# Performance work log

Measured on AMD Instinct MI355X. Metric: run time of the kernel, lower is better.

Reference implementation:

```python
import jax, jax.numpy as jnp
import numpy as np
import math

EMBED = 1024
HEADS = 16
HEAD_DIM = EMBED // HEADS  # 64
BSZ = 32
TGT = 512   # == src_len, required by the bmm-over-sequence structure
SRC = 512   # == BSZ*HEADS, required by the need_weights view


def _xavier(k, shape):
    fan_out, fan_in = shape
    limit = math.sqrt(6.0 / (fan_in + fan_out))
    return jax.random.uniform(k, shape, jnp.float32, -limit, limit)


def setup_inputs() -> dict:
    key = jax.random.key(0)
    ks = jax.random.split(key, 8)
    d = EMBED
    return {
        # query given as [bsz, tgt_len, d]; the module transposes it internally
        "query": jax.random.normal(ks[0], (BSZ, TGT, d), jnp.float32),
        "key": jax.random.normal(ks[1], (SRC, BSZ, d), jnp.float32),
        "value": jax.random.normal(ks[2], (SRC, BSZ, d), jnp.float32),
        "Wq": _xavier(ks[3], (d, d)), "bq": jnp.zeros((d,), jnp.float32),
        "Wk": _xavier(ks[4], (d, d)), "bk": jnp.zeros((d,), jnp.float32),
        "Wv": _xavier(ks[5], (d, d)), "bv": jnp.zeros((d,), jnp.float32),
        "Wo": _xavier(ks[6], (d, d)), "bo": jnp.zeros((d,), jnp.float32),
    }


def reference(query, key, value, Wq, bq, Wk, bk, Wv, bv, Wo, bo):
    H, hd = HEADS, HEAD_DIM
    # module transposes [bsz, tgt_len, d] -> [tgt_len, bsz, d]
    query = jnp.transpose(query, (1, 0, 2))
    T, B, D = query.shape
    S = key.shape[0]  # == T and == B*H by construction
    # projections (nn.Linear: x @ W.T + b)
    q = (query @ Wq.T + bq).reshape(T, B * H, hd)
    k = (key @ Wk.T + bk).reshape(S, B * H, hd)
    v = (value @ Wv.T + bv).reshape(S, B * H, hd)
    # torch.bmm with the SEQUENCE dim as the bmm batch dim (faithful to source):
    # scores: [T, BH, BH]
    scores = jnp.einsum('tbd,tcd->tbc', q, k) / jnp.sqrt(jnp.asarray(hd, q.dtype))
    attn = jax.nn.softmax(scores, axis=-1)  # dropout p=0.0, eval mode
    out = jnp.einsum('tbc,tcd->tbd', attn, v)  # [T, BH, hd]
    out = out.reshape(T, B, D) @ Wo.T + bo     # [T, B, D]
    # need_weights=True branch: view [T,H,B,S], permute(2,1,0,3), mean over heads
    w = attn.reshape(T, H, B, S).transpose(2, 1, 0, 3).mean(axis=1)  # [B, T, S]
    return out, w
```

## Files before the change

kernel.cpp:

```cpp
#include <hip/hip_runtime.h>
#include <hip/hip_bf16.h>
#include <stdint.h>


typedef __attribute__((ext_vector_type(8))) short bf16x8;
typedef __attribute__((ext_vector_type(4))) float f32x4;
typedef unsigned short u16;
typedef unsigned int u32;

typedef __attribute__((address_space(1))) const unsigned int as1_u32;
typedef __attribute__((address_space(3))) unsigned int as3_u32;

__device__ __forceinline__ void glds16(const void* g, void* l) {
    __builtin_amdgcn_global_load_lds((as1_u32*)g, (as3_u32*)l, 16, 0, 0);
}

__device__ __forceinline__ u16 f2bf(float f) {
    u32 u = __builtin_bit_cast(u32, f);
    u32 r = (u + 0x7FFFu + ((u >> 16) & 1u)) >> 16;
    return (u16)r;
}

template <int CTRL>
__device__ __forceinline__ float dpp_add(float x) {
    int xi = __builtin_bit_cast(int, x);
    int yi = __builtin_amdgcn_update_dpp(0, xi, CTRL, 0xF, 0xF, true);
    return x + __builtin_bit_cast(float, yi);
}
__device__ __forceinline__ float red16(float v) {
    v = dpp_add<0xB1>(v);
    v = dpp_add<0x4E>(v);
    v = dpp_add<0x141>(v);
    v = dpp_add<0x140>(v);
    return v;
}

__global__ void convw_kernel(const float4* __restrict__ query,
                             const float4* __restrict__ key,
                             const float4* __restrict__ value,
                             const float4* __restrict__ Wq, const float4* __restrict__ Wk,
                             const float4* __restrict__ Wv, const float4* __restrict__ Wo,
                             uint2* __restrict__ qx, uint2* __restrict__ kx,
                             uint2* __restrict__ vx,
                             uint2* __restrict__ wqb, uint2* __restrict__ wkb,
                             uint2* __restrict__ wvb, uint2* __restrict__ wob) {
    const int NT = gridDim.x * blockDim.x;
    for (int i = blockIdx.x * blockDim.x + threadIdx.x; i < 13631488; i += NT) {
        float4 v; uint2* d; int di;
        if (i < 4194304) {
            int m = i >> 8, c4 = i & 255;
            int t = m >> 5, b = m & 31;
            v = query[(b * 512 + t) * 256 + c4];
            d = qx; di = i;
        } else if (i < 8388608) {
            di = i - 4194304; v = key[di]; d = kx;
        } else if (i < 12582912) {
            di = i - 8388608; v = value[di]; d = vx;
        } else {
            int jj = i - 12582912;
            int wsel = jj >> 18; di = jj & 262143;
            const float4* s = wsel == 0 ? Wq : wsel == 1 ? Wk : wsel == 2 ? Wv : Wo;
            d = wsel == 0 ? wqb : wsel == 1 ? wkb : wsel == 2 ? wvb : wob;
            v = s[di];
        }
        uint2 r;
        r.x = (u32)f2bf(v.x) | ((u32)f2bf(v.y) << 16);
        r.y = (u32)f2bf(v.z) | ((u32)f2bf(v.w) << 16);
        d[di] = r;
    }
}

template <int F32OUT>
__global__ __launch_bounds__(256, 2)
void gemm_bb(const u16* __restrict__ A0, const u16* __restrict__ A1,
             const u16* __restrict__ A2,
             const u16* __restrict__ B0, const u16* __restrict__ B1,
             const u16* __restrict__ B2,
             const float* __restrict__ b0, const float* __restrict__ b1,
             const float* __restrict__ b2,
             void* __restrict__ C0, void* __restrict__ C1, void* __restrict__ C2) {
    __shared__ __align__(16) u16 As[2][8192];
    __shared__ __align__(16) u16 Bs[2][8192];
    const int z = blockIdx.z;
    const u16* A = z == 0 ? A0 : z == 1 ? A1 : A2;
    const u16* B = z == 0 ? B0 : z == 1 ? B1 : B2;
    const float* bias = z == 0 ? b0 : z == 1 ? b1 : b2;
    void* Cp = z == 0 ? C0 : z == 1 ? C1 : C2;
    const int tid = threadIdx.x;
    const int id = blockIdx.x;
    const int xcd = id & 7, j = id >> 3;
    const int ny = j & 7, band = xcd * 16 + (j >> 3);
    const long N0 = (long)ny * 128;
    const long M0 = (long)band * 128;
    const int lane = tid & 63, wv = tid >> 6;
    const int l15 = lane & 15, g = lane >> 4;
    const int wm = (wv >> 1) * 64, wn = (wv & 1) * 64;

    auto gldsAB = [&](int kt, int buf) {
#pragma unroll
        for (int i2 = 0; i2 < 4; ++i2) {
            int q = tid + 256 * i2; int r = q >> 3, c16 = q & 7;
            int c16s = c16 ^ (r & 7);
            char* lbA = (char*)As[buf] + (i2 * 256 + wv * 64) * 16;
            char* lbB = (char*)Bs[buf] + (i2 * 256 + wv * 64) * 16;
            glds16(A + (M0 + r) * 1024 + kt * 64 + c16s * 8, lbA);
            glds16(B + (N0 + r) * 1024 + kt * 64 + c16s * 8, lbB);
        }
    };
    gldsAB(0, 0);
    __syncthreads();
    f32x4 acc[4][4] = {};
    const int swz = (l15 & 7) << 4;
    for (int kt = 0; kt < 16; ++kt) {
        if (kt < 15) gldsAB(kt + 1, (kt + 1) & 1);
        const char* Acur = (const char*)As[kt & 1];
        const char* Bcur = (const char*)Bs[kt & 1];
#pragma unroll
        for (int kk = 0; kk < 2; ++kk) {
            bf16x8 av[4], bvv[4];
#pragma unroll
            for (int mt = 0; mt < 4; ++mt) {
                int row = wm + mt * 16 + l15;
                av[mt] = *(const bf16x8*)(Acur + row * 128 + ((kk * 64 + g * 16) ^ swz));
            }
#pragma unroll
            for (int nt = 0; nt < 4; ++nt) {
                int row = wn + nt * 16 + l15;
                bvv[nt] = *(const bf16x8*)(Bcur + row * 128 + ((kk * 64 + g * 16) ^ swz));
            }
#pragma unroll
            for (int mt = 0; mt < 4; ++mt)
#pragma unroll
                for (int nt = 0; nt < 4; ++nt)
                    acc[mt][nt] = __builtin_amdgcn_mfma_f32_16x16x32_bf16(av[mt], bvv[nt], acc[mt][nt], 0, 0, 0);
        }
        __syncthreads();
    }
    float bsv[4];
#pragma unroll
    for (int nt = 0; nt < 4; ++nt) bsv[nt] = bias[N0 + wn + nt * 16 + l15];
#pragma unroll
    for (int mt = 0; mt < 4; ++mt)
#pragma unroll
        for (int nt = 0; nt < 4; ++nt)
#pragma unroll
            for (int r = 0; r < 4; ++r) {
                long m = M0 + wm + mt * 16 + g * 4 + r;
                long n = N0 + wn + nt * 16 + l15;
                float v = acc[mt][nt][r] + bsv[nt];
                if (F32OUT) ((float*)Cp)[m * 1024 + n] = v;
                else        ((u16*)Cp)[m * 1024 + n] = f2bf(v);
            }
}

__global__ __launch_bounds__(512, 2)
void attn_kernel(const u16* __restrict__ Q, const u16* __restrict__ K,
                 const u16* __restrict__ V, u16* __restrict__ ctx,
                 float* __restrict__ wout) {
    __shared__ __align__(16) char smem[32768];
    const int bid = blockIdx.x;
    const int wk_ = (bid & 7) * 256 + (bid >> 3);
    const int t = wk_ >> 2, it = wk_ & 3;
    const int tid = threadIdx.x, lane = tid & 63, wv = tid >> 6;
    const int l15 = lane & 15, g = lane >> 4;
    const int swk = (l15 & 7) << 4;
    const int bb = it * 8 + wv;
    const float ksc = 0.18033688011112042f;

    const u16* Kt = K + (size_t)t * 32768;
    const u16* Vt = V + (size_t)t * 32768;

    auto stageK = [&](int q, int slot) {
#pragma unroll
        for (int hh = 0; hh < 2; ++hh) {
            int idx = hh * 512 + tid;
            int sl = idx >> 3, c16 = idx & 7;
            int csw = c16 ^ (sl & 7);
            glds16(Kt + (size_t)(q * 128 + sl) * 64 + csw * 8,
                   smem + slot * 16384 + hh * 8192 + wv * 1024);
        }
    };
    bf16x8 vreg[2];
    auto loadV = [&](int q) {
#pragma unroll
        for (int hh = 0; hh < 2; ++hh) {
            int u = hh * 512 + tid;
            int sl = u >> 3, ec = u & 7;
            vreg[hh] = *(const bf16x8*)(Vt + (size_t)(q * 128 + sl) * 64 + ec * 8);
        }
    };
    auto writeV = [&](int slot) {
        char* base = smem + slot * 16384;
#pragma unroll
        for (int hh = 0; hh < 2; ++hh) {
            int u = hh * 512 + tid;
            int sl = u >> 3, ec = u & 7;
#pragma unroll
            for (int jj = 0; jj < 8; ++jj) {
                int swv = (jj ^ (ec & 3)) << 4;
                *(u16*)(base + (ec * 8 + jj) * 256 + ((sl * 2) ^ swv)) = (u16)vreg[hh][jj];
            }
        }
    };
    f32x4 pv[4];
    auto pvQuarter = [&](const char* vb, bf16x8 p0, bf16x8 p1, bf16x8 p2, bf16x8 p3) {
        bf16x8 pq[4] = {p0, p1, p2, p3};
        __builtin_amdgcn_s_setprio(1);
#pragma unroll
        for (int m = 0; m < 4; ++m) {
#pragma unroll
            for (int nt = 0; nt < 4; ++nt) {
                int e = nt * 16 + l15;
                int esw = ((e & 7) ^ ((e >> 3) & 3)) << 4;
                const char* vrow = vb + e * 256;
                union { bf16x8 v; uint2 uu[2]; } bv;
                bv.uu[0] = *(const uint2*)(vrow + ((m * 64 + 8 * g) ^ esw));
                bv.uu[1] = *(const uint2*)(vrow + ((m * 64 + 32 + 8 * g) ^ esw));
                pv[nt] = __builtin_amdgcn_mfma_f32_16x16x32_bf16(pq[m], bv.v, pv[nt], 0, 0, 0);
            }
        }
        __builtin_amdgcn_s_setprio(0);
    };

    const int c = 32 * l15 + bb;
    const u16* qrow = Q + ((size_t)t * 512 + c) * 64;
    bf16x8 qb0 = *(const bf16x8*)(qrow + g * 8);
    bf16x8 qb1 = *(const bf16x8*)(qrow + 32 + g * 8);

    stageK(0, 0);
    __syncthreads();
    float sum = 0.f;
    bf16x8 pP[16];
#pragma unroll
    for (int q = 0; q < 4; ++q) {
        if (q < 3) stageK(q + 1, (q + 1) & 1);
        else loadV(0);
        const char* kb = smem + (q & 1) * 16384;
        __builtin_amdgcn_s_setprio(1);
#pragma unroll
        for (int m = 0; m < 4; ++m) {
            union { bf16x8 v; u32 u[4]; } pa;
#pragma unroll
            for (int h2 = 0; h2 < 2; ++h2) {
                int lsl = 2 * m + h2;
                const char* rowp = kb + (lsl * 16 + l15) * 128;
                bf16x8 a0 = *(const bf16x8*)(rowp + ((g * 16) ^ swk));
                bf16x8 a1 = *(const bf16x8*)(rowp + ((64 + g * 16) ^ swk));
                f32x4 zz = {0.f, 0.f, 0.f, 0.f};
                zz = __builtin_amdgcn_mfma_f32_16x16x32_bf16(a0, qb0, zz, 0, 0, 0);
                zz = __builtin_amdgcn_mfma_f32_16x16x32_bf16(a1, qb1, zz, 0, 0, 0);
                float e0 = exp2f(zz[0] * ksc), e1 = exp2f(zz[1] * ksc);
                float e2 = exp2f(zz[2] * ksc), e3 = exp2f(zz[3] * ksc);
                sum += (e0 + e1) + (e2 + e3);
                pa.u[2 * h2]     = (u32)f2bf(e0) | ((u32)f2bf(e1) << 16);
                pa.u[2 * h2 + 1] = (u32)f2bf(e2) | ((u32)f2bf(e3) << 16);
            }
            pP[q * 4 + m] = pa.v;
        }
        __builtin_amdgcn_s_setprio(0);
        __syncthreads();
    }
    sum += __shfl_xor(sum, 16);
    sum += __shfl_xor(sum, 32);
    const float inv = 1.f / sum;

    writeV(0);
    loadV(1);

    {
        const float inv16 = inv * 0.0625f;
        float4 wreg0 = {0.f, 0.f, 0.f, 0.f}, wreg1 = {0.f, 0.f, 0.f, 0.f};
#pragma unroll
        for (int st = 0; st < 32; ++st) {
            union { bf16x8 v; u32 u[4]; } pu; pu.v = pP[st >> 1];
            u32 ua = pu.u[(st & 1) * 2], ub = pu.u[(st & 1) * 2 + 1];
            float v0 = __builtin_bit_cast(float, (ua & 0xFFFFu) << 16) * inv16;
            float v1 = __builtin_bit_cast(float, ua & 0xFFFF0000u) * inv16;
            float v2 = __builtin_bit_cast(float, (ub & 0xFFFFu) << 16) * inv16;
            float v3 = __builtin_bit_cast(float, ub & 0xFFFF0000u) * inv16;
            v0 = red16(v0); v1 = red16(v1); v2 = red16(v2); v3 = red16(v3);
            if ((st >> 1) == l15) {
                if (st & 1) wreg1 = (float4){v0, v1, v2, v3};
                else        wreg0 = (float4){v0, v1, v2, v3};
            }
        }
        float* wrow = wout + ((size_t)(bb * 512 + t)) * 512 + 32 * l15 + 4 * g;
        *(float4*)(wrow) = wreg0;
        *(float4*)(wrow + 16) = wreg1;
    }
    __syncthreads();

#pragma unroll
    for (int nt = 0; nt < 4; ++nt) pv[nt] = (f32x4){0.f, 0.f, 0.f, 0.f};
    writeV(1);
    pvQuarter(smem, pP[0], pP[1], pP[2], pP[3]);
    loadV(2);
    __syncthreads();
    writeV(0);
    pvQuarter(smem + 16384, pP[4], pP[5], pP[6], pP[7]);
    loadV(3);
    __syncthreads();
    writeV(1);
    pvQuarter(smem, pP[8], pP[9], pP[10], pP[11]);
    __syncthreads();
    pvQuarter(smem + 16384, pP[12], pP[13], pP[14], pP[15]);

    float invv[4];
#pragma unroll
    for (int r = 0; r < 4; ++r) invv[r] = __shfl(inv, g * 4 + r);
#pragma unroll
    for (int nt = 0; nt < 4; ++nt)
#pragma unroll
        for (int r = 0; r < 4; ++r)
            ctx[((size_t)t * 512 + 32 * (g * 4 + r) + bb) * 64 + nt * 16 + l15] =
                f2bf(pv[nt][r] * invv[r]);
}

extern "C" void kernel_launch(void* const* d_in, const int* in_sizes, int n_in,
                              void* d_out, int out_size, void* d_ws, size_t ws_size,
                              hipStream_t stream) {
    const float* query = (const float*)d_in[0];
    const float* key   = (const float*)d_in[1];
    const float* value = (const float*)d_in[2];
    const float* Wq = (const float*)d_in[3];  const float* bq = (const float*)d_in[4];
    const float* Wk = (const float*)d_in[5];  const float* bk = (const float*)d_in[6];
    const float* Wv = (const float*)d_in[7];  const float* bv = (const float*)d_in[8];
    const float* Wo = (const float*)d_in[9];  const float* bo = (const float*)d_in[10];

    char* ws = (char*)d_ws;
    u16* wqb  = (u16*)(ws + 0);
    u16* wkb  = (u16*)(ws + 2097152);
    u16* wvb  = (u16*)(ws + 4194304);
    u16* wob  = (u16*)(ws + 6291456);
    u16* q_ws = (u16*)(ws + 8388608);
    u16* k_ws = (u16*)(ws + 41943040);
    u16* v_ws = (u16*)(ws + 75497472);
    u16* qx   = (u16*)(ws + 109051904);

    float* out  = (float*)d_out;
    float* wout = out + 16777216;
    u16* kx = (u16*)d_out;
    u16* vx = (u16*)((char*)d_out + 33554432);

    convw_kernel<<<2048, 256, 0, stream>>>(
        (const float4*)query, (const float4*)key, (const float4*)value,
        (const float4*)Wq, (const float4*)Wk, (const float4*)Wv, (const float4*)Wo,
        (uint2*)qx, (uint2*)kx, (uint2*)vx,
        (uint2*)wqb, (uint2*)wkb, (uint2*)wvb, (uint2*)wob);

    dim3 gg3(1024, 1, 3);
    gemm_bb<0><<<gg3, 256, 0, stream>>>(qx, kx, vx, wqb, wkb, wvb,
                                        bq, bk, bv, q_ws, k_ws, v_ws);

    attn_kernel<<<2048, 512, 0, stream>>>(q_ws, k_ws, v_ws, q_ws, wout);

    gemm_bb<1><<<dim3(1024, 1, 1), 256, 0, stream>>>(q_ws, q_ws, q_ws,
                                                     wob, wob, wob, bo, bo, bo,
                                                     out, out, out);
}
```

Baseline: 353.8 us.

## Pre-transpose V in a separate kernel and stage it via async LDS loads

Adds a kernel that transposes the V projection per sequence position into an [e][c] layout in a scratch region of the output buffer. The attention kernel can then stage V tiles with global_load_lds 16-byte copies, replacing the register load followed by scalar 2-byte scattered LDS writes, and the V-slot swizzle is simplified to match. The aim is to cut LDS write instruction count and register pressure in the attention kernel. In exchange it adds an extra kernel launch plus a full read and write of V (32 MB bf16) through global memory.

```diff
diff --git a/kernel.cpp b/kernel.cpp
--- a/kernel.cpp
+++ b/kernel.cpp
@@ -153,9 +153,33 @@
             }
 }
 
+__global__ __launch_bounds__(256)
+void vtrans_kernel(const u16* __restrict__ v_ws, u16* __restrict__ vt) {
+    __shared__ __align__(16) u16 tl[64][136];
+    const int bid = blockIdx.x;
+    const int t = bid >> 2, c0 = (bid & 3) * 128;
+    const u16* src = v_ws + (size_t)t * 32768 + (size_t)c0 * 64;
+#pragma unroll
+    for (int i = 0; i < 4; ++i) {
+        int ch = i * 256 + threadIdx.x;
+        int rc = ch >> 3, e0 = (ch & 7) * 8;
+        bf16x8 v8 = *(const bf16x8*)(src + rc * 64 + e0);
+#pragma unroll
+        for (int j = 0; j < 8; ++j) tl[e0 + j][rc] = (u16)v8[j];
+    }
+    __syncthreads();
+    u16* dst = vt + (size_t)t * 32768 + c0;
+#pragma unroll
+    for (int i = 0; i < 4; ++i) {
+        int ch = i * 256 + threadIdx.x;
+        int e = ch >> 4, cc = (ch & 15) * 8;
+        *(bf16x8*)(dst + (size_t)e * 512 + cc) = *(const bf16x8*)(&tl[e][cc]);
+    }
+}
+
 __global__ __launch_bounds__(512, 2)
 void attn_kernel(const u16* __restrict__ Q, const u16* __restrict__ K,
-                 const u16* __restrict__ V, u16* __restrict__ ctx,
+                 const u16* __restrict__ VT, u16* __restrict__ ctx,
                  float* __restrict__ wout) {
     __shared__ __align__(16) char smem[32768];
     const int bid = blockIdx.x;
@@ -168,7 +192,7 @@
     const float ksc = 0.18033688011112042f;
 
     const u16* Kt = K + (size_t)t * 32768;
-    const u16* Vt = V + (size_t)t * 32768;
+    const u16* Vtt = VT + (size_t)t * 32768;
 
     auto stageK = [&](int q, int slot) {
 #pragma unroll
@@ -180,26 +204,13 @@
                    smem + slot * 16384 + hh * 8192 + wv * 1024);
         }
     };
-    bf16x8 vreg[2];
-    auto loadV = [&](int q) {
+    auto stageV = [&](int q, int slot) {
 #pragma unroll
         for (int hh = 0; hh < 2; ++hh) {
-            int u = hh * 512 + tid;
-            int sl = u >> 3, ec = u & 7;
-            vreg[hh] = *(const bf16x8*)(Vt + (size_t)(q * 128 + sl) * 64 + ec * 8);
-        }
-    };
-    auto writeV = [&](int slot) {
-        char* base = smem + slot * 16384;
-#pragma unroll
-        for (int hh = 0; hh < 2; ++hh) {
-            int u = hh * 512 + tid;
-            int sl = u >> 3, ec = u & 7;
-#pragma unroll
-            for (int jj = 0; jj < 8; ++jj) {
-                int swv = (jj ^ (ec & 3)) << 4;
-                *(u16*)(base + (ec * 8 + jj) * 256 + ((sl * 2) ^ swv)) = (u16)vreg[hh][jj];
-            }
+            int ch = hh * 512 + tid;
+            int e = ch >> 4, c16 = ch & 15;
+            glds16(Vtt + (size_t)e * 512 + q * 128 + ((c16 ^ (e & 7)) << 3),
+                   smem + slot * 16384 + hh * 8192 + wv * 1024);
         }
     };
     f32x4 pv[4];
@@ -211,7 +222,7 @@
 #pragma unroll
             for (int nt = 0; nt < 4; ++nt) {
                 int e = nt * 16 + l15;
-                int esw = ((e & 7) ^ ((e >> 3) & 3)) << 4;
+                int esw = (e & 7) << 4;
                 const char* vrow = vb + e * 256;
                 union { bf16x8 v; uint2 uu[2]; } bv;
                 bv.uu[0] = *(const uint2*)(vrow + ((m * 64 + 8 * g) ^ esw));
@@ -234,7 +245,7 @@
 #pragma unroll
     for (int q = 0; q < 4; ++q) {
         if (q < 3) stageK(q + 1, (q + 1) & 1);
-        else loadV(0);
+        else stageV(0, 0);
         const char* kb = smem + (q & 1) * 16384;
         __builtin_amdgcn_s_setprio(1);
 #pragma unroll
@@ -264,8 +275,7 @@
     sum += __shfl_xor(sum, 32);
     const float inv = 1.f / sum;
 
-    writeV(0);
-    loadV(1);
+    stageV(1, 1);
 
     {
         const float inv16 = inv * 0.0625f;
@@ -292,15 +302,12 @@
 
 #pragma unroll
     for (int nt = 0; nt < 4; ++nt) pv[nt] = (f32x4){0.f, 0.f, 0.f, 0.f};
-    writeV(1);
     pvQuarter(smem, pP[0], pP[1], pP[2], pP[3]);
-    loadV(2);
-    __syncthreads();
-    writeV(0);
+    __syncthreads();
+    stageV(2, 0);
     pvQuarter(smem + 16384, pP[4], pP[5], pP[6], pP[7]);
-    loadV(3);
-    __syncthreads();
-    writeV(1);
+    __syncthreads();
+    stageV(3, 1);
     pvQuarter(smem, pP[8], pP[9], pP[10], pP[11]);
     __syncthreads();
     pvQuarter(smem + 16384, pP[12], pP[13], pP[14], pP[15]);
@@ -341,6 +348,7 @@
     float* wout = out + 16777216;
     u16* kx = (u16*)d_out;
     u16* vx = (u16*)((char*)d_out + 33554432);
+    u16* vt = (u16*)((char*)d_out + 33554432);
 
     convw_kernel<<<2048, 256, 0, stream>>>(
         (const float4*)query, (const float4*)key, (const float4*)value,
@@ -352,7 +360,9 @@
     gemm_bb<0><<<gg3, 256, 0, stream>>>(qx, kx, vx, wqb, wkb, wvb,
                                         bq, bk, bv, q_ws, k_ws, v_ws);
 
-    attn_kernel<<<2048, 512, 0, stream>>>(q_ws, k_ws, v_ws, q_ws, wout);
+    vtrans_kernel<<<2048, 256, 0, stream>>>(v_ws, vt);
+
+    attn_kernel<<<2048, 512, 0, stream>>>(q_ws, k_ws, vt, q_ws, wout);
 
     gemm_bb<1><<<dim3(1024, 1, 1), 256, 0, stream>>>(q_ws, q_ws, q_ws,
                                                      wob, wob, wob, bo, bo, bo,
```

New measurement: 372.4 us. 1.05x slower.
